# Kernel tuning notes

Hardware: AMD Instinct MI355X
Metric: run time of the kernel (lower is better)

## Reference

```python
import jax, jax.numpy as jnp
import numpy as np

EPS = 1e-5
B, C, H, W, K = 4, 512, 128, 128, 32


def setup_inputs() -> dict:
    key = jax.random.key(0)
    ks = jax.random.split(key, 12)
    std = 1.0 / ((K * C) ** 0.5)
    return {
        "x": jax.random.normal(ks[0], (B, C, H, W), jnp.float32),
        "conv_w": jax.random.normal(ks[1], (C, C), jnp.float32) * (1.0 / C ** 0.5),
        "bn2_g": jnp.ones((C,), jnp.float32),
        "bn2_b": jnp.zeros((C,), jnp.float32),
        "bn2_m": jax.random.normal(ks[2], (C,), jnp.float32) * 0.1,
        "bn2_v": jax.random.uniform(ks[3], (C,), jnp.float32) + 0.5,
        "codewords": jax.random.uniform(ks[4], (K, C), jnp.float32, -std, std),
        "scale": jax.random.uniform(ks[5], (K,), jnp.float32, -1.0, 0.0),
        "bn1_g": jnp.ones((K,), jnp.float32),
        "bn1_b": jnp.zeros((K,), jnp.float32),
        "bn1_m": jax.random.normal(ks[6], (K,), jnp.float32) * 0.1,
        "bn1_v": jax.random.uniform(ks[7], (K,), jnp.float32) + 0.5,
        "fc_w": jax.random.normal(ks[8], (C, C), jnp.float32) * (1.0 / C ** 0.5),
        "fc_b": jnp.zeros((C,), jnp.float32),
    }


def _encoding(z, codewords, scale):
    # z: [B,N,C], codewords: [K,C], scale: [K]
    # scaled L2: scale_k * ||z_n - c_k||^2, expanded to avoid the [B,N,K,C] tensor
    x2 = jnp.sum(z * z, axis=-1, keepdims=True)          # [B,N,1]
    c2 = jnp.sum(codewords * codewords, axis=-1)         # [K]
    xc = jnp.einsum('bnc,kc->bnk', z, codewords)         # [B,N,K]
    scaled_l2 = scale * (x2 - 2.0 * xc + c2)             # [B,N,K]
    assign = jax.nn.softmax(scaled_l2, axis=-1)          # softmax over codes
    # aggregate: sum_n assign[b,n,k] * (z[b,n,:] - c[k,:])
    agg = jnp.einsum('bnk,bnc->bkc', assign, z) \
        - jnp.sum(assign, axis=1)[..., None] * codewords  # [B,K,C]
    return agg


def reference(x, conv_w, bn2_g, bn2_b, bn2_m, bn2_v, codewords, scale,
              bn1_g, bn1_b, bn1_m, bn1_v, fc_w, fc_b):
    b, c, h, w = x.shape
    # encoding_project: 1x1 conv (no bias) + BN2d (eval) + ReLU
    p = jnp.einsum('bchw,oc->bohw', x, conv_w)
    p = (p - bn2_m[None, :, None, None]) * jax.lax.rsqrt(bn2_v + EPS)[None, :, None, None] \
        * bn2_g[None, :, None, None] + bn2_b[None, :, None, None]
    p = jax.nn.relu(p)
    z = p.reshape(b, c, h * w).transpose(0, 2, 1)        # [B,N,C]
    e = _encoding(z, codewords, scale)                   # [B,K,C]
    # BN1d over num_codes (eval), broadcast over channel dim, then ReLU
    e = (e - bn1_m[None, :, None]) * jax.lax.rsqrt(bn1_v + EPS)[None, :, None] \
        * bn1_g[None, :, None] + bn1_b[None, :, None]
    e = jax.nn.relu(e)
    feat = e.mean(axis=1)                                # [B,C]
    gamma = jax.nn.sigmoid(feat @ fc_w.T + fc_b)         # [B,C]
    out = jax.nn.relu(x + x * gamma[:, :, None, None])   # channel gate + residual
    return feat, out
```

## Files before the change

### kernel.cpp

```cpp
#include <hip/hip_runtime.h>
#include <cstdint>

#define EPS 1e-5f
constexpr int B = 4, C = 512, HW = 16384, K = 32;

typedef __bf16 bf16x8 __attribute__((ext_vector_type(8)));
typedef float  floatx4 __attribute__((ext_vector_type(4)));
typedef unsigned int u32;

__device__ __forceinline__ void load_lds16(const void* g, void* l) {
    __builtin_amdgcn_global_load_lds((const __attribute__((address_space(1))) u32*)g,
                                     (__attribute__((address_space(3))) u32*)l,
                                     16, 0, 0);
}

constexpr size_t Z_OFF     = 0;
constexpr size_t WBB_OFF   = 67108864;
constexpr size_t CWB_OFF   = 67633152;
constexpr size_t X2_OFF    = 67665920;
constexpr size_t C2_OFF    = 67928064;
constexpr size_t ASUM_OFF  = 67928192;
constexpr size_t PART_OFF  = 67928704;
constexpr size_t AGG_OFF   = 101483136;
constexpr size_t GAMMA_OFF = 101745280;

__global__ __launch_bounds__(256) void prep_kernel(
    const float* __restrict__ conv_w, const float* __restrict__ cw,
    __bf16* __restrict__ wbb, __bf16* __restrict__ cwb,
    float* __restrict__ c2, float* __restrict__ asum) {
    const int tid = threadIdx.x;
    if (blockIdx.x < 68) {
        int idx = (blockIdx.x * 256 + tid) * 16;
        const float* s;
        __bf16* d;
        if (idx < 262144) { s = conv_w + idx; d = wbb + idx; }
        else              { s = cw + (idx - 262144); d = cwb + (idx - 262144); }
        bf16x8 o0, o1;
        #pragma unroll
        for (int j = 0; j < 8; j++) o0[j] = (__bf16)s[j];
        #pragma unroll
        for (int j = 0; j < 8; j++) o1[j] = (__bf16)s[8 + j];
        *(bf16x8*)&d[0] = o0;
        *(bf16x8*)&d[8] = o1;
    } else {
        if (tid < 32) {
            const float* r = cw + tid * 512;
            float s = 0.f;
            for (int c = 0; c < 512; c++) s += r[c] * r[c];
            c2[tid] = s;
        }
        if (tid < 128) asum[tid] = 0.f;
    }
}

__global__ __launch_bounds__(256) void conv_fused_kernel(
    const float* __restrict__ x, const __bf16* __restrict__ wbb,
    const float* __restrict__ g2, const float* __restrict__ b2,
    const float* __restrict__ m2, const float* __restrict__ v2,
    __bf16* __restrict__ z, float* __restrict__ x2g) {
    __shared__ float  XR[2][64 * 64];
    __shared__ __bf16 XA[2][64 * 72];
    __shared__ float  x2L[64];
    const int tid = threadIdx.x, lane = tid & 63, w = tid >> 6;
    const int l15 = lane & 15, q = lane >> 4;
    const int n0 = blockIdx.x * 64, b = blockIdx.y;
    if (tid < 64) x2L[tid] = 0.f;

    auto stage = [&](int chunk, int buf) {
        #pragma unroll
        for (int p = 0; p < 4; p++) {
            int seg = w * 4 + p;
            int cr = chunk * 64 + seg * 4 + (lane >> 4);
            const float* gp = x + ((size_t)(b * C + cr)) * HW + n0 + (lane & 15) * 4;
            load_lds16(gp, (char*)XR[buf] + seg * 1024);
        }
    };

    floatx4 acc[4][8];
    const floatx4 zv4 = {0.f, 0.f, 0.f, 0.f};
    #pragma unroll
    for (int mt = 0; mt < 4; mt++)
        #pragma unroll
        for (int ot = 0; ot < 8; ot++) acc[mt][ot] = zv4;

    stage(0, 0);
    for (int i = 0; i < 8; i++) {
        const int buf = i & 1;
        __syncthreads();
        if (i < 7) stage(i + 1, buf ^ 1);
        #pragma unroll
        for (int f = 0; f < 2; f++) {
            int id = f * 256 + tid;
            int n = id & 63, cs = id >> 6;
            bf16x8 o;
            #pragma unroll
            for (int j = 0; j < 8; j++) o[j] = (__bf16)XR[buf][(cs * 8 + j) * 64 + n];
            *(bf16x8*)&XA[buf][n * 72 + cs * 8] = o;
        }
        __syncthreads();
        #pragma unroll
        for (int ks = 0; ks < 2; ks++) {
            bf16x8 af[4], bfv[8];
            #pragma unroll
            for (int mt = 0; mt < 4; mt++)
                af[mt] = *(const bf16x8*)&XA[buf][(mt * 16 + l15) * 72 + ks * 32 + q * 8];
            #pragma unroll
            for (int ot = 0; ot < 8; ot++)
                bfv[ot] = *(const bf16x8*)&wbb[(size_t)(w * 128 + ot * 16 + l15) * C
                                               + i * 64 + ks * 32 + q * 8];
            #pragma unroll
            for (int mt = 0; mt < 4; mt++)
                #pragma unroll
                for (int ot = 0; ot < 8; ot++)
                    acc[mt][ot] = __builtin_amdgcn_mfma_f32_16x16x32_bf16(
                        af[mt], bfv[ot], acc[mt][ot], 0, 0, 0);
        }
    }
    float s8[8], bi8[8];
    #pragma unroll
    for (int ot = 0; ot < 8; ot++) {
        int o = w * 128 + ot * 16 + l15;
        float s = g2[o] * rsqrtf(v2[o] + EPS);
        s8[ot] = s; bi8[ot] = b2[o] - m2[o] * s;
    }
    float xx[16];
    #pragma unroll
    for (int t = 0; t < 16; t++) xx[t] = 0.f;
    #pragma unroll
    for (int mt = 0; mt < 4; mt++)
        #pragma unroll
        for (int reg = 0; reg < 4; reg++) {
            int n = n0 + mt * 16 + q * 4 + reg;
            #pragma unroll
            for (int ot = 0; ot < 8; ot++) {
                float v = fmaxf(acc[mt][ot][reg] * s8[ot] + bi8[ot], 0.f);
                z[((size_t)(b * HW + n)) * C + w * 128 + ot * 16 + l15] = (__bf16)v;
                xx[mt * 4 + reg] += v * v;
            }
        }
    #pragma unroll
    for (int t = 0; t < 16; t++) {
        float v = xx[t];
        v += __shfl_xor(v, 1); v += __shfl_xor(v, 2);
        v += __shfl_xor(v, 4); v += __shfl_xor(v, 8);
        xx[t] = v;
    }
    if (l15 == 0) {
        #pragma unroll
        for (int mt = 0; mt < 4; mt++)
            #pragma unroll
            for (int reg = 0; reg < 4; reg++)
                atomicAdd(&x2L[mt * 16 + q * 4 + reg], xx[mt * 4 + reg]);
    }
    __syncthreads();
    if (tid < 64) x2g[(size_t)b * HW + n0 + tid] = x2L[tid];
}

__global__ __launch_bounds__(256) void assign_agg_kernel(
    const __bf16* __restrict__ zb, const __bf16* __restrict__ cwb,
    const float* __restrict__ scale, const float* __restrict__ c2,
    const float* __restrict__ x2g, float* __restrict__ part,
    float* __restrict__ asum) {
    __shared__ __bf16 ZT[32][528];
    __shared__ float  LG[32][33];
    __shared__ __bf16 AT[32][40];
    __shared__ float  asum_l[32];
    const int tid = threadIdx.x, lane = tid & 63, w = tid >> 6;
    const int l15 = lane & 15, q = lane >> 4;
    const int b = blockIdx.y, bx = blockIdx.x;
    if (tid < 32) asum_l[tid] = 0.f;
    float sck[8], c2k[8];
    #pragma unroll
    for (int j = 0; j < 8; j++) { sck[j] = scale[q * 8 + j]; c2k[j] = c2[q * 8 + j]; }
    const int mt_ = w >> 1, nt_ = w & 1;

    floatx4 agga[2][8];
    const floatx4 zv4 = {0.f, 0.f, 0.f, 0.f};
    #pragma unroll
    for (int mt = 0; mt < 2; mt++)
        #pragma unroll
        for (int ct = 0; ct < 8; ct++) agga[mt][ct] = zv4;

    for (int s = 0; s < 4; s++) {
        const int nb = bx * 128 + s * 32;
        bf16x8 st[8];
        #pragma unroll
        for (int p = 0; p < 8; p++) {
            int e = (p * 256 + tid) * 8;
            int n = e >> 9, c = e & 511;
            st[p] = *(const bf16x8*)&zb[((size_t)(b * HW + nb + n)) * C + c];
        }
        __syncthreads();
        #pragma unroll
        for (int p = 0; p < 8; p++) {
            int e = (p * 256 + tid) * 8;
            int n = e >> 9, c = e & 511;
            *(bf16x8*)&ZT[n][c] = st[p];
        }
        __syncthreads();
        floatx4 la = zv4;
        #pragma unroll
        for (int kc = 0; kc < 16; kc++) {
            bf16x8 a  = *(const bf16x8*)&cwb[(size_t)(mt_ * 16 + l15) * C + kc * 32 + q * 8];
            bf16x8 bb = *(const bf16x8*)&ZT[nt_ * 16 + l15][kc * 32 + q * 8];
            la = __builtin_amdgcn_mfma_f32_16x16x32_bf16(a, bb, la, 0, 0, 0);
        }
        #pragma unroll
        for (int r = 0; r < 4; r++)
            LG[mt_ * 16 + q * 4 + r][nt_ * 16 + l15] = la[r];
        __syncthreads();
        if (w < 2) {
            int nl = w * 16 + l15;
            float x2v = x2g[(size_t)b * HW + nb + nl];
            float lg[8];
            float mx = -1e30f;
            #pragma unroll
            for (int j = 0; j < 8; j++) {
                float t = sck[j] * (x2v - 2.f * LG[q * 8 + j][nl] + c2k[j]);
                lg[j] = t; mx = fmaxf(mx, t);
            }
            mx = fmaxf(mx, __shfl_xor(mx, 16));
            mx = fmaxf(mx, __shfl_xor(mx, 32));
            float se = 0.f;
            #pragma unroll
            for (int j = 0; j < 8; j++) { lg[j] = __expf(lg[j] - mx); se += lg[j]; }
            se += __shfl_xor(se, 16);
            se += __shfl_xor(se, 32);
            float inv = 1.f / se;
            #pragma unroll
            for (int j = 0; j < 8; j++) {
                float a = lg[j] * inv;
                AT[q * 8 + j][nl] = (__bf16)a;
                lg[j] = a;
            }
            #pragma unroll
            for (int j = 0; j < 8; j++) {
                float v = lg[j];
                v += __shfl_xor(v, 1); v += __shfl_xor(v, 2);
                v += __shfl_xor(v, 4); v += __shfl_xor(v, 8);
                if (l15 == 0) atomicAdd(&asum_l[q * 8 + j], v);
            }
        }
        __syncthreads();
        bf16x8 afr0 = *(const bf16x8*)&AT[l15][q * 8];
        bf16x8 afr1 = *(const bf16x8*)&AT[16 + l15][q * 8];
        #pragma unroll
        for (int ct = 0; ct < 8; ct++) {
            int c = w * 128 + ct * 16 + l15;
            bf16x8 bb;
            #pragma unroll
            for (int j = 0; j < 8; j++) bb[j] = ZT[q * 8 + j][c];
            agga[0][ct] = __builtin_amdgcn_mfma_f32_16x16x32_bf16(afr0, bb, agga[0][ct], 0, 0, 0);
            agga[1][ct] = __builtin_amdgcn_mfma_f32_16x16x32_bf16(afr1, bb, agga[1][ct], 0, 0, 0);
        }
    }
    float* pp = part + ((size_t)(b * 128 + bx) * K) * C;
    #pragma unroll
    for (int mt = 0; mt < 2; mt++)
        #pragma unroll
        for (int ct = 0; ct < 8; ct++)
            #pragma unroll
            for (int r = 0; r < 4; r++)
                pp[(size_t)(mt * 16 + q * 4 + r) * C + w * 128 + ct * 16 + l15] =
                    agga[mt][ct][r];
    __syncthreads();
    if (tid < 32) atomicAdd(&asum[b * K + tid], asum_l[tid]);
}

__global__ __launch_bounds__(512) void agg_reduce_kernel(
    const float* __restrict__ part, float* __restrict__ agg) {
    const int k = blockIdx.x, b = blockIdx.y, c = threadIdx.x;
    float s = 0.f;
    for (int p = 0; p < 128; p++)
        s += part[((size_t)((b * 128 + p) * K + k)) * C + c];
    agg[((size_t)(b * K + k)) * C + c] = s;
}

__global__ __launch_bounds__(512) void feat_kernel(
    const float* __restrict__ cw,
    const float* __restrict__ g1, const float* __restrict__ b1,
    const float* __restrict__ m1, const float* __restrict__ v1,
    const float* __restrict__ fcw, const float* __restrict__ fcb,
    const float* __restrict__ agg, const float* __restrict__ asum,
    float* __restrict__ gamma, float* __restrict__ out_feat) {
    __shared__ float featL[C];
    const int tid = threadIdx.x;
    const int b = blockIdx.x;
    float f = 0.f;
    for (int kk = 0; kk < K; kk++) {
        float s = g1[kk] * rsqrtf(v1[kk] + EPS);
        float bias = b1[kk] - m1[kk] * s;
        float e = agg[((size_t)b * K + kk) * C + tid] - asum[b * K + kk] * cw[kk * C + tid];
        f += fmaxf(e * s + bias, 0.f);
    }
    f *= (1.f / 32.f);
    out_feat[b * C + tid] = f;
    featL[tid] = f;
    __syncthreads();
    const int w = tid >> 6, l = tid & 63;
    for (int cc = w * 64; cc < w * 64 + 64; cc++) {
        const float* row = &fcw[(size_t)cc * C + l * 8];
        float4 fa = *(const float4*)&featL[l * 8];
        float4 fb = *(const float4*)&featL[l * 8 + 4];
        float4 wa = *(const float4*)row;
        float4 wb = *(const float4*)(row + 4);
        float s = fa.x * wa.x + fa.y * wa.y + fa.z * wa.z + fa.w * wa.w
                + fb.x * wb.x + fb.y * wb.y + fb.z * wb.z + fb.w * wb.w;
        #pragma unroll
        for (int d = 32; d >= 1; d >>= 1) s += __shfl_xor(s, d);
        if (l == 0) gamma[b * C + cc] = 1.f / (1.f + __expf(-(s + fcb[cc])));
    }
}

__global__ __launch_bounds__(256) void gate_kernel(const float* __restrict__ x,
                                                   const float* __restrict__ gamma,
                                                   float* __restrict__ out) {
    size_t idx = (size_t)blockIdx.x * 256 + threadIdx.x;
    int bc = (int)(idx >> 12);
    float gm = 1.f + gamma[bc];
    float4 xv = ((const float4*)x)[idx];
    float4 r;
    r.x = fmaxf(xv.x * gm, 0.f);
    r.y = fmaxf(xv.y * gm, 0.f);
    r.z = fmaxf(xv.z * gm, 0.f);
    r.w = fmaxf(xv.w * gm, 0.f);
    ((float4*)out)[idx] = r;
}

extern "C" void kernel_launch(void* const* d_in, const int* in_sizes, int n_in,
                              void* d_out, int out_size, void* d_ws, size_t ws_size,
                              hipStream_t stream) {
    const float* x      = (const float*)d_in[0];
    const float* conv_w = (const float*)d_in[1];
    const float* bn2_g  = (const float*)d_in[2];
    const float* bn2_b  = (const float*)d_in[3];
    const float* bn2_m  = (const float*)d_in[4];
    const float* bn2_v  = (const float*)d_in[5];
    const float* cw     = (const float*)d_in[6];
    const float* scale  = (const float*)d_in[7];
    const float* bn1_g  = (const float*)d_in[8];
    const float* bn1_b  = (const float*)d_in[9];
    const float* bn1_m  = (const float*)d_in[10];
    const float* bn1_v  = (const float*)d_in[11];
    const float* fcw    = (const float*)d_in[12];
    const float* fcb    = (const float*)d_in[13];
    char* wsb = (char*)d_ws;
    __bf16* zbuf  = (__bf16*)(wsb + Z_OFF);
    __bf16* wbb   = (__bf16*)(wsb + WBB_OFF);
    __bf16* cwb   = (__bf16*)(wsb + CWB_OFF);
    float*  x2    = (float*)(wsb + X2_OFF);
    float*  c2    = (float*)(wsb + C2_OFF);
    float*  asum  = (float*)(wsb + ASUM_OFF);
    float*  part  = (float*)(wsb + PART_OFF);
    float*  agg   = (float*)(wsb + AGG_OFF);
    float*  gamma = (float*)(wsb + GAMMA_OFF);
    float* out = (float*)d_out;

    prep_kernel<<<69, 256, 0, stream>>>(conv_w, cw, wbb, cwb, c2, asum);
    conv_fused_kernel<<<dim3(256, 4), 256, 0, stream>>>(
        x, wbb, bn2_g, bn2_b, bn2_m, bn2_v, zbuf, x2);
    assign_agg_kernel<<<dim3(128, 4), 256, 0, stream>>>(
        zbuf, cwb, scale, c2, x2, part, asum);
    agg_reduce_kernel<<<dim3(32, 4), 512, 0, stream>>>(part, agg);
    feat_kernel<<<4, 512, 0, stream>>>(cw, bn1_g, bn1_b, bn1_m, bn1_v,
                                       fcw, fcb, agg, asum, gamma, out);
    gate_kernel<<<32768, 256, 0, stream>>>(x, gamma, out + B * C);
}
```

Baseline: 477.5 us.

## Pre-swizzle conv weights into MFMA fragment order and single-buffer the bf16 LDS tile

The prep kernel now writes the bf16 conv weights in per-lane MFMA B-fragment order. Each lane in the conv kernel then reads a contiguous 16-byte chunk, replacing row-strided global loads. The bf16 activation LDS tile is reduced from double to single buffering, which lowers LDS use. The second __syncthreads is replaced by an explicit lgkmcnt wait plus s_barrier fenced with sched_barriers, so the compiler cannot reorder loads across it. The cost is a larger prep launch and more fragile hand-written synchronisation.

```diff
diff --git a/kernel.cpp b/kernel.cpp
--- a/kernel.cpp
+++ b/kernel.cpp
@@ -28,13 +28,23 @@
     const float* __restrict__ conv_w, const float* __restrict__ cw,
     __bf16* __restrict__ wbb, __bf16* __restrict__ cwb,
     float* __restrict__ c2, float* __restrict__ asum) {
-    const int tid = threadIdx.x;
-    if (blockIdx.x < 68) {
-        int idx = (blockIdx.x * 256 + tid) * 16;
-        const float* s;
-        __bf16* d;
-        if (idx < 262144) { s = conv_w + idx; d = wbb + idx; }
-        else              { s = cw + (idx - 262144); d = cwb + (idx - 262144); }
+    const int tid = threadIdx.x, bx = blockIdx.x;
+    if (bx < 128) {
+        const int idx  = bx * 256 + tid;
+        const int lane = idx & 63;
+        const int ks   = (idx >> 6) & 1;
+        const int ii   = (idx >> 7) & 7;
+        const int t    = idx >> 10;
+        const float* s = conv_w + (size_t)(t * 16 + (lane & 15)) * C
+                         + ii * 64 + ks * 32 + (lane >> 4) * 8;
+        bf16x8 o;
+        #pragma unroll
+        for (int j = 0; j < 8; j++) o[j] = (__bf16)s[j];
+        *(bf16x8*)&wbb[(size_t)idx * 8] = o;
+    } else if (bx < 132) {
+        const int idx = ((bx - 128) * 256 + tid) * 16;
+        const float* s = cw + idx;
+        __bf16* d = cwb + idx;
         bf16x8 o0, o1;
         #pragma unroll
         for (int j = 0; j < 8; j++) o0[j] = (__bf16)s[j];
@@ -59,7 +69,7 @@
     const float* __restrict__ m2, const float* __restrict__ v2,
     __bf16* __restrict__ z, float* __restrict__ x2g) {
     __shared__ float  XR[2][64 * 64];
-    __shared__ __bf16 XA[2][64 * 72];
+    __shared__ __bf16 XA[64 * 72];
     __shared__ float  x2L[64];
     const int tid = threadIdx.x, lane = tid & 63, w = tid >> 6;
     const int l15 = lane & 15, q = lane >> 4;
@@ -85,29 +95,32 @@
 
     stage(0, 0);
     for (int i = 0; i < 8; i++) {
-        const int buf = i & 1;
-        __syncthreads();
-        if (i < 7) stage(i + 1, buf ^ 1);
+        const int cur = i & 1;
+        __syncthreads();
+        if (i < 7) stage(i + 1, cur ^ 1);
         #pragma unroll
         for (int f = 0; f < 2; f++) {
             int id = f * 256 + tid;
             int n = id & 63, cs = id >> 6;
             bf16x8 o;
             #pragma unroll
-            for (int j = 0; j < 8; j++) o[j] = (__bf16)XR[buf][(cs * 8 + j) * 64 + n];
-            *(bf16x8*)&XA[buf][n * 72 + cs * 8] = o;
-        }
-        __syncthreads();
+            for (int j = 0; j < 8; j++) o[j] = (__bf16)XR[cur][(cs * 8 + j) * 64 + n];
+            *(bf16x8*)&XA[n * 72 + cs * 8] = o;
+        }
+        asm volatile("s_waitcnt lgkmcnt(0)" ::: "memory");
+        __builtin_amdgcn_sched_barrier(0);
+        __builtin_amdgcn_s_barrier();
+        __builtin_amdgcn_sched_barrier(0);
         #pragma unroll
         for (int ks = 0; ks < 2; ks++) {
             bf16x8 af[4], bfv[8];
             #pragma unroll
+            for (int ot = 0; ot < 8; ot++)
+                bfv[ot] = *(const bf16x8*)&wbb[
+                    ((size_t)(((w * 8 + ot) * 8 + i) * 2 + ks) * 64 + lane) * 8];
+            #pragma unroll
             for (int mt = 0; mt < 4; mt++)
-                af[mt] = *(const bf16x8*)&XA[buf][(mt * 16 + l15) * 72 + ks * 32 + q * 8];
-            #pragma unroll
-            for (int ot = 0; ot < 8; ot++)
-                bfv[ot] = *(const bf16x8*)&wbb[(size_t)(w * 128 + ot * 16 + l15) * C
-                                               + i * 64 + ks * 32 + q * 8];
+                af[mt] = *(const bf16x8*)&XA[(mt * 16 + l15) * 72 + ks * 32 + q * 8];
             #pragma unroll
             for (int mt = 0; mt < 4; mt++)
                 #pragma unroll
@@ -356,7 +369,7 @@
     float*  gamma = (float*)(wsb + GAMMA_OFF);
     float* out = (float*)d_out;
 
-    prep_kernel<<<69, 256, 0, stream>>>(conv_w, cw, wbb, cwb, c2, asum);
+    prep_kernel<<<133, 256, 0, stream>>>(conv_w, cw, wbb, cwb, c2, asum);
     conv_fused_kernel<<<dim3(256, 4), 256, 0, stream>>>(
         x, wbb, bn2_g, bn2_b, bn2_m, bn2_v, zbuf, x2);
     assign_agg_kernel<<<dim3(128, 4), 256, 0, stream>>>(
```

New measurement: 448.9 us. -6.0%, faster.
